# Kernel tuning notes

Measured on AMD Instinct MI355X. Metric: run time of the kernel, lower is better.

Reference implementation:

```python
import jax, jax.numpy as jnp
import numpy as np

N_NODES = 10000
N_EDGES = 160000
D = 128        # embedding_dim = in/out channels
E_DIM = 32     # edge feature dim
HEADS = 3
N_ETYPES = 64
ROUNDS = 2     # num_message_rounds
NEG_SLOPE = 0.2


def _lookup_maxnorm(table, idx):
    # torch Embedding(max_norm=1): rows with L2 norm > 1 are renormalized to norm 1
    v = table[idx]
    n = jnp.linalg.norm(v, axis=-1, keepdims=True)
    return v / jnp.maximum(n, 1.0)


def _edge_gat(x, src, dst, edge_attr, weight, att, euw, bias):
    # x: [N, D]; src/dst: [E] (self loops included); edge_attr: [E, E_DIM]
    N = x.shape[0]
    H = HEADS
    C = weight.shape[1] // H
    xh = (x @ weight).reshape(N, H, C)                 # [N, H, C]
    x_j = xh[src]                                      # gather source nodes  [E, H, C]
    x_i = xh[dst]                                      # gather target nodes  [E, H, C]
    ea = jnp.broadcast_to(edge_attr[:, None, :], (src.shape[0], H, edge_attr.shape[-1]))
    xj_cat = jnp.concatenate([x_j, ea], axis=-1)       # [E, H, C+E_DIM]
    # attention logits: (cat(x_i, x_j, e) * att).sum(-1)
    alpha = jnp.sum(jnp.concatenate([x_i, xj_cat], axis=-1) * att, axis=-1)  # [E, H]
    alpha = jax.nn.leaky_relu(alpha, NEG_SLOPE)
    # scatter-softmax over incoming edges of each dst node (stable)
    m = jax.ops.segment_max(alpha, dst, num_segments=N)        # [N, H]
    a = jnp.exp(alpha - m[dst])
    denom = jax.ops.segment_sum(a, dst, num_segments=N)        # [N, H]
    a = a / denom[dst]
    # weighted scatter-add aggregate
    aggr = jax.ops.segment_sum(xj_cat * a[..., None], dst, num_segments=N)  # [N, H, C+E_DIM]
    return aggr.mean(axis=1) @ euw + bias                       # [N, C]


def setup_inputs() -> dict:
    key = jax.random.key(0)
    ks = jax.random.split(key, 13)
    x_idx = jnp.arange(N_NODES, dtype=jnp.int32)
    src = jax.random.randint(ks[0], (N_EDGES,), 0, N_NODES, dtype=jnp.int32)
    off = jax.random.randint(ks[1], (N_EDGES,), 1, N_NODES, dtype=jnp.int32)
    dst = (src + off) % N_NODES    # guaranteed self-loop-free
    edge_index = jnp.stack([src, dst])
    edge_attr_idx = jax.random.randint(ks[2], (N_EDGES,), 0, N_ETYPES, dtype=jnp.int32)
    def g(k, shape):
        return jax.random.normal(k, shape, jnp.float32) * np.float32(np.sqrt(2.0 / sum(shape)))
    node_emb = g(ks[3], (N_NODES, D))
    edge_emb = g(ks[4], (N_ETYPES, E_DIM))
    w1 = g(ks[5], (D, HEADS * D))
    att1 = g(ks[6], (1, HEADS, 2 * D + E_DIM))
    euw1 = g(ks[7], (D + E_DIM, D))
    b1 = jnp.zeros((D,), jnp.float32)
    w2 = g(ks[8], (D, HEADS * D))
    att2 = g(ks[9], (1, HEADS, 2 * D + E_DIM))
    euw2 = g(ks[10], (D + E_DIM, D))
    b2 = jnp.zeros((D,), jnp.float32)
    return dict(x_idx=x_idx, edge_index=edge_index, edge_attr_idx=edge_attr_idx,
                node_emb=node_emb, edge_emb=edge_emb,
                w1=w1, att1=att1, euw1=euw1, b1=b1,
                w2=w2, att2=att2, euw2=euw2, b2=b2)


def reference(x_idx, edge_index, edge_attr_idx, node_emb, edge_emb,
              w1, att1, euw1, b1, w2, att2, euw2, b2):
    N = node_emb.shape[0]
    src0, dst0 = edge_index[0], edge_index[1]
    loop = jnp.arange(N, dtype=src0.dtype)
    src = jnp.concatenate([src0, loop])
    dst = jnp.concatenate([dst0, loop])
    x = _lookup_maxnorm(node_emb, x_idx)               # [N, D]
    ea = edge_emb[edge_attr_idx]                       # [E0, E_DIM]
    ea_full = jnp.concatenate([ea, jnp.zeros((N, ea.shape[-1]), ea.dtype)], axis=0)
    for _ in range(ROUNDS):
        # eval mode: dropout is identity
        x = jax.nn.elu(_edge_gat(x, src, dst, ea_full, w1, att1, euw1, b1))
        x = _edge_gat(x, src, dst, ea_full, w2, att2, euw2, b2)
    return x
```

## Files before the change

kernel.cpp:

```cpp
#include <hip/hip_runtime.h>
#include <hip/hip_bf16.h>

typedef __hip_bfloat16 bf16;
typedef __attribute__((ext_vector_type(8))) short short8;
typedef __attribute__((ext_vector_type(4))) float f32x4;

__device__ __forceinline__ float b2f(bf16 v) { return __bfloat162float(v); }
__device__ __forceinline__ float2 i2f2(int w) {
  float lo = __uint_as_float(((unsigned)w) << 16);
  float hi = __uint_as_float(((unsigned)w) & 0xFFFF0000u);
  return make_float2(lo, hi);
}
__device__ __forceinline__ unsigned f2bfb(float f) {
  unsigned u = __float_as_uint(f);
  unsigned r = 0x7FFFu + ((u >> 16) & 1u);
  return (u + r) >> 16;
}
__device__ __forceinline__ unsigned pk2(float a, float b) {
  return f2bfb(a) | (f2bfb(b) << 16);
}
__device__ __forceinline__ float ldv(const void* p, int i, int f) {
  return f ? ((const float*)p)[i] : b2f(((const bf16*)p)[i]);
}

__global__ __launch_bounds__(512) void detect_set_kernel(
    const unsigned short* __restrict__ probe, int nhalves, int* __restrict__ flag,
    const void* __restrict__ eeraw, const void* __restrict__ att1raw,
    const void* __restrict__ att2raw, float* __restrict__ s_et) {
  __shared__ int cnt;
  __shared__ int fl;
  if (threadIdx.x == 0) cnt = 0;
  __syncthreads();
  int local = 0;
  for (int i = threadIdx.x; i < nhalves; i += 512) {
    int e = (probe[i] >> 7) & 0xFF;
    if (e >= 160) local++;
  }
  if (local) atomicAdd(&cnt, local);
  __syncthreads();
  if (threadIdx.x == 0) { fl = (cnt > 16) ? 1 : 0; *flag = fl; }
  __syncthreads();
  int f = fl;
  int id = threadIdx.x;
  if (id < 2 * 65 * 3) {
    int l = id / (65 * 3);
    int r = id % (65 * 3);
    int t = r / 3, h = r % 3;
    const void* att = l ? att2raw : att1raw;
    float s = 0.0f;
    if (t < 64) {
      for (int d = 0; d < 32; ++d)
        s += ldv(eeraw, t * 32 + d, f) * ldv(att, h * 288 + 256 + d, f);
    }
    s_et[id] = s;
  }
}

__global__ __launch_bounds__(256) void wconv_kernel(
    const void* __restrict__ ee, const void* __restrict__ w1,
    const void* __restrict__ a1, const void* __restrict__ eu1,
    const void* __restrict__ b1, const void* __restrict__ w2,
    const void* __restrict__ a2, const void* __restrict__ eu2,
    const void* __restrict__ b2, const int* __restrict__ flag,
    float* __restrict__ eef, float* __restrict__ att1f, float* __restrict__ att2f,
    float* __restrict__ b1f, float* __restrict__ b2f,
    bf16* __restrict__ WT1, bf16* __restrict__ WT2,
    bf16* __restrict__ euT1, bf16* __restrict__ euT2,
    int* __restrict__ counts, int N) {
  int i = blockIdx.x * 256 + threadIdx.x;
  int f = *flag;
  if (i < 2048) {
    eef[i] = ldv(ee, i, f);
  } else if (i < 2912) {
    att1f[i - 2048] = ldv(a1, i - 2048, f);
  } else if (i < 3776) {
    att2f[i - 2912] = ldv(a2, i - 2912, f);
  } else if (i < 3904) {
    b1f[i - 3776] = ldv(b1, i - 3776, f);
  } else if (i < 4032) {
    b2f[i - 3904] = ldv(b2, i - 3904, f);
  } else if (i < 53184) {
    int j = i - 4032; int c = j >> 7, k = j & 127;
    WT1[j] = __float2bfloat16(ldv(w1, k * 384 + c, f));
  } else if (i < 102336) {
    int j = i - 53184; int c = j >> 7, k = j & 127;
    WT2[j] = __float2bfloat16(ldv(w2, k * 384 + c, f));
  } else if (i < 122816) {
    int j = i - 102336; int c = j / 160, k = j % 160;
    euT1[j] = __float2bfloat16(ldv(eu1, k * 128 + c, f));
  } else if (i < 143296) {
    int j = i - 122816; int c = j / 160, k = j % 160;
    euT2[j] = __float2bfloat16(ldv(eu2, k * 128 + c, f));
  } else if (i < 143296 + N) {
    counts[i - 143296] = 0;
  }
}

__global__ __launch_bounds__(256) void prep_kernel(
    const int* __restrict__ x_idx, const void* __restrict__ node_emb,
    const int* __restrict__ flag, bf16* __restrict__ xb,
    int* __restrict__ counts, const int* __restrict__ dst, int E0, int N) {
  int wid = threadIdx.x >> 6, lane = threadIdx.x & 63;
  int n = blockIdx.x * 4 + wid;
  if (n < N) {
    int idx = x_idx[n];
    if ((unsigned)idx >= (unsigned)N) idx = 0;
    float v0, v1;
    if (*flag) {
      const float* er = (const float*)node_emb + (size_t)idx * 128;
      v0 = er[lane]; v1 = er[lane + 64];
    } else {
      const bf16* er = (const bf16*)node_emb + (size_t)idx * 128;
      v0 = b2f(er[lane]); v1 = b2f(er[lane + 64]);
    }
    float ss = v0 * v0 + v1 * v1;
#pragma unroll
    for (int d = 32; d > 0; d >>= 1) ss += __shfl_xor(ss, d);
    float norm = sqrtf(ss);
    float scale = norm > 1.0f ? 1.0f / norm : 1.0f;
    xb[(size_t)n * 128 + lane] = __float2bfloat16(v0 * scale);
    xb[(size_t)n * 128 + 64 + lane] = __float2bfloat16(v1 * scale);
  }
  int gid = blockIdx.x * 256 + threadIdx.x;
  int stride = gridDim.x * 256;
  for (int i = gid; i < E0; i += stride) {
    int d = dst[i];
    if ((unsigned)d >= (unsigned)N) d = 0;
    atomicAdd(&counts[d], 1);
  }
}

__global__ __launch_bounds__(64) void scan_kernel(
    int* __restrict__ counts, int* __restrict__ row_ptr, int N) {
  int lane = threadIdx.x;
  int chunk = (N + 63) / 64;
  int lo = lane * chunk;
  int hi = lo + chunk; if (hi > N) hi = N; if (lo > N) lo = N;
  int s = 0;
  for (int i = lo; i < hi; ++i) s += counts[i] + 1;
  int incl = s;
#pragma unroll
  for (int d = 1; d < 64; d <<= 1) {
    int t = __shfl_up(incl, d);
    if (lane >= d) incl += t;
  }
  int run = incl - s;
  for (int i = lo; i < hi; ++i) {
    int c = counts[i] + 1;
    row_ptr[i] = run;
    counts[i] = run;
    run += c;
  }
  if (lane == 63) row_ptr[N] = run;
}

__global__ __launch_bounds__(256) void scatter_kernel(
    const int* __restrict__ src, const int* __restrict__ dst,
    const int* __restrict__ et, int* __restrict__ cursor,
    int* __restrict__ packed, int E0, int N) {
  int E = E0 + N;
  int i = blockIdx.x * blockDim.x + threadIdx.x;
  if (i < E0) {
    int d = dst[i];
    if ((unsigned)d >= (unsigned)N) d = 0;
    int p = atomicAdd(&cursor[d], 1);
    if ((unsigned)p >= (unsigned)E) p = 0;
    int t = et[i] & 63;
    packed[p] = (src[i] & 0xFFFF) | (t << 16);
  } else if (i < E) {
    int n = i - E0;
    int p = atomicAdd(&cursor[n], 1);
    if ((unsigned)p >= (unsigned)E) p = 0;
    packed[p] = (n & 0xFFFF) | (64 << 16);
  }
}

__global__ __launch_bounds__(256) void gemm_xh_mfma(
    const bf16* __restrict__ x, const bf16* __restrict__ WT,
    bf16* __restrict__ xh, int N) {
  int wave = threadIdx.x >> 6, lane = threadIdx.x & 63;
  int row_base = blockIdx.x * 16;
  int col_base = blockIdx.y * 64 + wave * 16;
  int quad = lane >> 4, r16 = lane & 15;
  int row = row_base + r16; if (row >= N) row = N - 1;
  int col = col_base + r16;
  f32x4 acc = {0.f, 0.f, 0.f, 0.f};
  const short8* ap = (const short8*)(x + (size_t)row * 128 + quad * 8);
  const short8* bp = (const short8*)(WT + (size_t)col * 128 + quad * 8);
#pragma unroll
  for (int kk = 0; kk < 4; ++kk) {
    short8 a = ap[kk * 4];
    short8 b = bp[kk * 4];
    acc = __builtin_amdgcn_mfma_f32_16x16x32_bf16(a, b, acc, 0, 0, 0);
  }
  int h = col >> 7, fi = col & 127, pair = fi >> 1, sub = fi & 1;
  size_t base = (size_t)pair * 6 + h * 2 + sub;
#pragma unroll
  for (int r = 0; r < 4; ++r) {
    int node = row_base + quad * 4 + r;
    if (node < N) xh[(size_t)node * 384 + base] = __float2bfloat16(acc[r]);
  }
}

__global__ __launch_bounds__(256) void s_kernel(
    const int* __restrict__ xh_i, const float2* __restrict__ attf2,
    float* __restrict__ s_i, float* __restrict__ s_j, int N) {
  int wid = threadIdx.x >> 6, lane = threadIdx.x & 63;
  int n = blockIdx.x * 4 + wid;
  if (n >= N) return;
  const int* p = xh_i + (size_t)n * 192 + lane * 3;
  int w0 = p[0], w1 = p[1], w2 = p[2];
  float2 v[3] = {i2f2(w0), i2f2(w1), i2f2(w2)};
#pragma unroll
  for (int h = 0; h < 3; ++h) {
    float2 ai = attf2[h * 144 + lane];
    float2 aj = attf2[h * 144 + 64 + lane];
    float pi = v[h].x * ai.x + v[h].y * ai.y;
    float pj = v[h].x * aj.x + v[h].y * aj.y;
#pragma unroll
    for (int d = 32; d > 0; d >>= 1) {
      pi += __shfl_xor(pi, d);
      pj += __shfl_xor(pj, d);
    }
    if (lane == 0) {
      s_i[n * 3 + h] = pi;
      s_j[n * 3 + h] = pj;
    }
  }
}

__global__ __launch_bounds__(256) void edge_aggr_kernel(
    const int* __restrict__ xh_i, const float* __restrict__ s_i,
    const float* __restrict__ s_j, const float* __restrict__ s_et,
    const float2* __restrict__ eef2, const int* __restrict__ row_ptr,
    const int* __restrict__ packed, unsigned* __restrict__ aggr_u,
    int N, int E) {
  int wid = threadIdx.x >> 6, lane = threadIdx.x & 63;
  int n = blockIdx.x * 4 + wid;
  if (n >= N) return;
  int start = row_ptr[n], end = row_ptr[n + 1];
  if (start < 0) start = 0;
  if (start > E) start = E;
  if (end < start) end = start;
  if (end > E) end = E;
  int deg = end - start;
  float si0 = s_i[n * 3 + 0], si1 = s_i[n * 3 + 1], si2 = s_i[n * 3 + 2];

  float p0r[2], p1r[2], p2r[2];
  int pkr[2];
  float dp0 = 0.0f, dp1 = 0.0f, dp2 = 0.0f;
#pragma unroll
  for (int it = 0; it < 2; ++it) {
    p0r[it] = p1r[it] = p2r[it] = 0.0f; pkr[it] = 0;
    int slot = it * 64 + lane;
    if (slot < deg) {
      int p = packed[start + slot];
      int s = p & 0xFFFF; if (s >= N) s = N - 1;
      int t = (p >> 16) & 127; if (t > 64) t = 64;
      float a0 = si0 + s_j[s * 3 + 0] + s_et[t * 3 + 0];
      float a1 = si1 + s_j[s * 3 + 1] + s_et[t * 3 + 1];
      float a2 = si2 + s_j[s * 3 + 2] + s_et[t * 3 + 2];
      a0 = a0 > 0.0f ? a0 : 0.2f * a0;
      a1 = a1 > 0.0f ? a1 : 0.2f * a1;
      a2 = a2 > 0.0f ? a2 : 0.2f * a2;
      a0 = fminf(fmaxf(a0, -60.0f), 60.0f);
      a1 = fminf(fmaxf(a1, -60.0f), 60.0f);
      a2 = fminf(fmaxf(a2, -60.0f), 60.0f);
      float p0 = __expf(a0), p1 = __expf(a1), p2 = __expf(a2);
      dp0 += p0; dp1 += p1; dp2 += p2;
      p0r[it] = p0; p1r[it] = p1; p2r[it] = p2;
      pkr[it] = s | (t << 16);
    }
  }
#pragma unroll
  for (int d = 32; d > 0; d >>= 1) {
    dp0 += __shfl_xor(dp0, d);
    dp1 += __shfl_xor(dp1, d);
    dp2 += __shfl_xor(dp2, d);
  }
  float d0 = dp0, d1 = dp1, d2 = dp2;

  float2 ax0 = make_float2(0.f, 0.f), ax1 = ax0, ax2 = ax0;
  float2 ae0 = ax0, ae1 = ax0, ae2 = ax0;
  int mm = deg < 128 ? deg : 128;

  auto agg_range = [&](int pk_s, float q0_s, float q1_s, float q2_s, int cnt) {
    int j = 0;
    for (; j + 2 <= cnt; j += 2) {
      int pkA = __shfl(pk_s, j), pkB = __shfl(pk_s, j + 1);
      float qA0 = __shfl(q0_s, j), qB0 = __shfl(q0_s, j + 1);
      float qA1 = __shfl(q1_s, j), qB1 = __shfl(q1_s, j + 1);
      float qA2 = __shfl(q2_s, j), qB2 = __shfl(q2_s, j + 1);
      int sA = pkA & 0xFFFF, tA = pkA >> 16;
      int sB = pkB & 0xFFFF, tB = pkB >> 16;
      const int* xpA = xh_i + (size_t)sA * 192 + lane * 3;
      const int* xpB = xh_i + (size_t)sB * 192 + lane * 3;
      int wA0 = xpA[0], wA1 = xpA[1], wA2 = xpA[2];
      int wB0 = xpB[0], wB1 = xpB[1], wB2 = xpB[2];
      float2 vA0 = i2f2(wA0), vA1 = i2f2(wA1), vA2 = i2f2(wA2);
      float2 vB0 = i2f2(wB0), vB1 = i2f2(wB1), vB2 = i2f2(wB2);
      ax0.x = fmaf(qA0, vA0.x, ax0.x); ax0.y = fmaf(qA0, vA0.y, ax0.y);
      ax1.x = fmaf(qA1, vA1.x, ax1.x); ax1.y = fmaf(qA1, vA1.y, ax1.y);
      ax2.x = fmaf(qA2, vA2.x, ax2.x); ax2.y = fmaf(qA2, vA2.y, ax2.y);
      ax0.x = fmaf(qB0, vB0.x, ax0.x); ax0.y = fmaf(qB0, vB0.y, ax0.y);
      ax1.x = fmaf(qB1, vB1.x, ax1.x); ax1.y = fmaf(qB1, vB1.y, ax1.y);
      ax2.x = fmaf(qB2, vB2.x, ax2.x); ax2.y = fmaf(qB2, vB2.y, ax2.y);
      if (lane < 16) {
        if (tA != 64) {
          float2 ev = eef2[tA * 16 + lane];
          ae0.x = fmaf(qA0, ev.x, ae0.x); ae0.y = fmaf(qA0, ev.y, ae0.y);
          ae1.x = fmaf(qA1, ev.x, ae1.x); ae1.y = fmaf(qA1, ev.y, ae1.y);
          ae2.x = fmaf(qA2, ev.x, ae2.x); ae2.y = fmaf(qA2, ev.y, ae2.y);
        }
        if (tB != 64) {
          float2 ev = eef2[tB * 16 + lane];
          ae0.x = fmaf(qB0, ev.x, ae0.x); ae0.y = fmaf(qB0, ev.y, ae0.y);
          ae1.x = fmaf(qB1, ev.x, ae1.x); ae1.y = fmaf(qB1, ev.y, ae1.y);
          ae2.x = fmaf(qB2, ev.x, ae2.x); ae2.y = fmaf(qB2, ev.y, ae2.y);
        }
      }
    }
    if (j < cnt) {
      int pkA = __shfl(pk_s, j);
      float qA0 = __shfl(q0_s, j), qA1 = __shfl(q1_s, j), qA2 = __shfl(q2_s, j);
      int sA = pkA & 0xFFFF, tA = pkA >> 16;
      const int* xpA = xh_i + (size_t)sA * 192 + lane * 3;
      int wA0 = xpA[0], wA1 = xpA[1], wA2 = xpA[2];
      float2 vA0 = i2f2(wA0), vA1 = i2f2(wA1), vA2 = i2f2(wA2);
      ax0.x = fmaf(qA0, vA0.x, ax0.x); ax0.y = fmaf(qA0, vA0.y, ax0.y);
      ax1.x = fmaf(qA1, vA1.x, ax1.x); ax1.y = fmaf(qA1, vA1.y, ax1.y);
      ax2.x = fmaf(qA2, vA2.x, ax2.x); ax2.y = fmaf(qA2, vA2.y, ax2.y);
      if (lane < 16 && tA != 64) {
        float2 ev = eef2[tA * 16 + lane];
        ae0.x = fmaf(qA0, ev.x, ae0.x); ae0.y = fmaf(qA0, ev.y, ae0.y);
        ae1.x = fmaf(qA1, ev.x, ae1.x); ae1.y = fmaf(qA1, ev.y, ae1.y);
        ae2.x = fmaf(qA2, ev.x, ae2.x); ae2.y = fmaf(qA2, ev.y, ae2.y);
      }
    }
  };
  agg_range(pkr[0], p0r[0], p1r[0], p2r[0], mm < 64 ? mm : 64);
  if (mm > 64) agg_range(pkr[1], p0r[1], p1r[1], p2r[1], mm - 64);

  for (int e = start + 128; e < end; ++e) {
    int p = packed[e];
    int s = p & 0xFFFF; if (s >= N) s = N - 1;
    int t = (p >> 16) & 127; if (t > 64) t = 64;
    float a0 = si0 + s_j[s * 3 + 0] + s_et[t * 3 + 0];
    float a1 = si1 + s_j[s * 3 + 1] + s_et[t * 3 + 1];
    float a2 = si2 + s_j[s * 3 + 2] + s_et[t * 3 + 2];
    a0 = a0 > 0.0f ? a0 : 0.2f * a0;
    a1 = a1 > 0.0f ? a1 : 0.2f * a1;
    a2 = a2 > 0.0f ? a2 : 0.2f * a2;
    a0 = fminf(fmaxf(a0, -60.0f), 60.0f);
    a1 = fminf(fmaxf(a1, -60.0f), 60.0f);
    a2 = fminf(fmaxf(a2, -60.0f), 60.0f);
    float p0 = __expf(a0), p1 = __expf(a1), p2 = __expf(a2);
    d0 += p0; d1 += p1; d2 += p2;
    const int* xp = xh_i + (size_t)s * 192 + lane * 3;
    float2 v0 = i2f2(xp[0]), v1 = i2f2(xp[1]), v2 = i2f2(xp[2]);
    ax0.x = fmaf(p0, v0.x, ax0.x); ax0.y = fmaf(p0, v0.y, ax0.y);
    ax1.x = fmaf(p1, v1.x, ax1.x); ax1.y = fmaf(p1, v1.y, ax1.y);
    ax2.x = fmaf(p2, v2.x, ax2.x); ax2.y = fmaf(p2, v2.y, ax2.y);
    if (t != 64 && lane < 16) {
      float2 ev = eef2[t * 16 + lane];
      ae0.x = fmaf(p0, ev.x, ae0.x); ae0.y = fmaf(p0, ev.y, ae0.y);
      ae1.x = fmaf(p1, ev.x, ae1.x); ae1.y = fmaf(p1, ev.y, ae1.y);
      ae2.x = fmaf(p2, ev.x, ae2.x); ae2.y = fmaf(p2, ev.y, ae2.y);
    }
  }

  const float third = 1.0f / 3.0f;
  float i0 = third / fmaxf(d0, 1e-30f);
  float i1 = third / fmaxf(d1, 1e-30f);
  float i2 = third / fmaxf(d2, 1e-30f);
  aggr_u[(size_t)n * 80 + lane] =
      pk2(ax0.x * i0 + ax1.x * i1 + ax2.x * i2,
          ax0.y * i0 + ax1.y * i1 + ax2.y * i2);
  if (lane < 16)
    aggr_u[(size_t)n * 80 + 64 + lane] =
        pk2(ae0.x * i0 + ae1.x * i1 + ae2.x * i2,
            ae0.y * i0 + ae1.y * i1 + ae2.y * i2);
}

__global__ __launch_bounds__(256) void gemm_out_mfma(
    const bf16* __restrict__ aggr, const bf16* __restrict__ euwT,
    const float* __restrict__ biasf, bf16* __restrict__ xb,
    void* __restrict__ dout, const int* __restrict__ flag,
    int N, int do_elu, int do_final) {
  int wave = threadIdx.x >> 6, lane = threadIdx.x & 63;
  int row_base = blockIdx.x * 16;
  int col_base = blockIdx.y * 64 + wave * 16;
  int quad = lane >> 4, r16 = lane & 15;
  int row = row_base + r16; if (row >= N) row = N - 1;
  int col = col_base + r16;
  f32x4 acc = {0.f, 0.f, 0.f, 0.f};
  const short8* ap = (const short8*)(aggr + (size_t)row * 160 + quad * 8);
  const short8* bp = (const short8*)(euwT + (size_t)col * 160 + quad * 8);
#pragma unroll
  for (int kk = 0; kk < 5; ++kk) {
    short8 a = ap[kk * 4];
    short8 b = bp[kk * 4];
    acc = __builtin_amdgcn_mfma_f32_16x16x32_bf16(a, b, acc, 0, 0, 0);
  }
  float bv = biasf[col];
  int f = *flag;
#pragma unroll
  for (int r = 0; r < 4; ++r) {
    int node = row_base + quad * 4 + r;
    if (node < N) {
      float v = acc[r] + bv;
      if (do_elu) v = v > 0.0f ? v : expm1f(v);
      if (do_final) {
        if (f) ((float*)dout)[(size_t)node * 128 + col] = v;
        else   ((bf16*)dout)[(size_t)node * 128 + col] = __float2bfloat16(v);
      } else {
        xb[(size_t)node * 128 + col] = __float2bfloat16(v);
      }
    }
  }
}

extern "C" void kernel_launch(void* const* d_in, const int* in_sizes, int n_in,
                              void* d_out, int out_size, void* d_ws, size_t ws_size,
                              hipStream_t stream) {
  const int* x_idx = (const int*)d_in[0];
  const int* edge_index = (const int*)d_in[1];
  const int* edge_attr_idx = (const int*)d_in[2];

  int N = in_sizes[0];
  int E0 = in_sizes[1] / 2;
  int E = E0 + N;
  const int* src = edge_index;
  const int* dst = edge_index + E0;

  size_t off = 0;
  char* base = (char*)d_ws;
  auto carve = [&](size_t bytes) -> void* {
    void* p = base + off;
    off += (bytes + 255) & ~(size_t)255;
    return p;
  };
  int* flag     = (int*)carve(256);
  int* counts   = (int*)carve((size_t)N * 4);
  int* row_ptr  = (int*)carve((size_t)(N + 1) * 4);
  int* packed   = (int*)carve((size_t)E * 4);
  float* s_i    = (float*)carve((size_t)N * 3 * 4);
  float* s_j    = (float*)carve((size_t)N * 3 * 4);
  float* s_et   = (float*)carve(2 * 65 * 3 * 4);
  float* eef    = (float*)carve(2048 * 4);
  float* att1f  = (float*)carve(864 * 4);
  float* att2f  = (float*)carve(864 * 4);
  float* b1f    = (float*)carve(128 * 4);
  float* b2f_   = (float*)carve(128 * 4);
  bf16* WT1     = (bf16*)carve(49152 * 2);
  bf16* WT2     = (bf16*)carve(49152 * 2);
  bf16* euT1    = (bf16*)carve(20480 * 2);
  bf16* euT2    = (bf16*)carve(20480 * 2);
  bf16* xh      = (bf16*)carve((size_t)N * 384 * 2 + 64);
  bf16* aggr    = (bf16*)carve((size_t)N * 160 * 2);
  bf16* xb      = (bf16*)d_out;
  (void)n_in; (void)out_size; (void)ws_size;

  detect_set_kernel<<<1, 512, 0, stream>>>(
      (const unsigned short*)d_in[5], 2048, flag, d_in[4], d_in[6], d_in[10], s_et);
  wconv_kernel<<<(143296 + N + 255) / 256, 256, 0, stream>>>(
      d_in[4], d_in[5], d_in[6], d_in[7], d_in[8], d_in[9], d_in[10], d_in[11],
      d_in[12], flag, eef, att1f, att2f, b1f, b2f_, WT1, WT2, euT1, euT2,
      counts, N);
  int nb4 = (N + 3) / 4;
  prep_kernel<<<nb4, 256, 0, stream>>>(x_idx, d_in[3], flag, xb, counts, dst,
                                       E0, N);
  scan_kernel<<<1, 64, 0, stream>>>(counts, row_ptr, N);
  scatter_kernel<<<(E + 255) / 256, 256, 0, stream>>>(src, dst, edge_attr_idx,
                                                      counts, packed, E0, N);

  const bf16* WTs[2] = {WT1, WT2};
  const float* atts[2] = {att1f, att2f};
  const bf16* euTs[2] = {euT1, euT2};
  const float* bs[2] = {b1f, b2f_};

  int nrb = (N + 15) / 16;
  for (int round = 0; round < 2; ++round) {
    for (int l = 0; l < 2; ++l) {
      int do_elu = (l == 0) ? 1 : 0;
      int do_final = (round == 1 && l == 1) ? 1 : 0;
      gemm_xh_mfma<<<dim3(nrb, 6), 256, 0, stream>>>(xb, WTs[l], xh, N);
      s_kernel<<<nb4, 256, 0, stream>>>((const int*)xh, (const float2*)atts[l],
                                        s_i, s_j, N);
      edge_aggr_kernel<<<nb4, 256, 0, stream>>>(
          (const int*)xh, s_i, s_j, s_et + l * 195, (const float2*)eef,
          row_ptr, packed, (unsigned*)aggr, N, E);
      gemm_out_mfma<<<dim3(nrb, 2), 256, 0, stream>>>(
          aggr, euTs[l], bs[l], xb, d_out, flag, N, do_elu, do_final);
    }
  }
}
```

Measured before the change: 382.0 us.

## Fuse attention score computation into xh GEMM and widen scan to 1024 threads

Merges the per-node attention dot products (s_i, s_j) into the xh projection GEMM epilogue, computing partial sums from MFMA accumulators and reducing via shuffles and LDS. This removes a separate kernel launch and a re-read of xh per layer. It also parallelizes the single-block prefix scan from 64 to 1024 threads with a two-level wave scan. The GEMM now uses one 384-thread block per 16 rows, which gives fewer blocks and lower parallelism, and it computes the scores from fp32 accumulators rather than the rounded bf16 values.

```diff
diff --git a/kernel.cpp b/kernel.cpp
--- a/kernel.cpp
+++ b/kernel.cpp
@@ -130,28 +130,40 @@
   }
 }
 
-__global__ __launch_bounds__(64) void scan_kernel(
+__global__ __launch_bounds__(1024) void scan_kernel(
     int* __restrict__ counts, int* __restrict__ row_ptr, int N) {
-  int lane = threadIdx.x;
-  int chunk = (N + 63) / 64;
-  int lo = lane * chunk;
-  int hi = lo + chunk; if (hi > N) hi = N; if (lo > N) lo = N;
+  __shared__ int wsum[16];
+  int t = threadIdx.x;
+  int chunk = (N + 1023) >> 10;
+  int lo = t * chunk;
+  int hi = lo + chunk;
+  if (lo > N) lo = N;
+  if (hi > N) hi = N;
   int s = 0;
   for (int i = lo; i < hi; ++i) s += counts[i] + 1;
+  int lane = t & 63, wv = t >> 6;
   int incl = s;
 #pragma unroll
   for (int d = 1; d < 64; d <<= 1) {
-    int t = __shfl_up(incl, d);
-    if (lane >= d) incl += t;
-  }
-  int run = incl - s;
+    int u = __shfl_up(incl, d);
+    if (lane >= d) incl += u;
+  }
+  if (lane == 63) wsum[wv] = incl;
+  __syncthreads();
+  if (t == 0) {
+    int run = 0;
+#pragma unroll
+    for (int w = 0; w < 16; ++w) { int c = wsum[w]; wsum[w] = run; run += c; }
+  }
+  __syncthreads();
+  int run = incl - s + wsum[wv];
   for (int i = lo; i < hi; ++i) {
     int c = counts[i] + 1;
     row_ptr[i] = run;
     counts[i] = run;
     run += c;
   }
-  if (lane == 63) row_ptr[N] = run;
+  if (t == 1023) row_ptr[N] = run;
 }
 
 __global__ __launch_bounds__(256) void scatter_kernel(
@@ -175,57 +187,72 @@
   }
 }
 
-__global__ __launch_bounds__(256) void gemm_xh_mfma(
+__global__ __launch_bounds__(384) void gemm_xh_s_mfma(
     const bf16* __restrict__ x, const bf16* __restrict__ WT,
-    bf16* __restrict__ xh, int N) {
+    const float* __restrict__ attf, bf16* __restrict__ xh,
+    float* __restrict__ s_i, float* __restrict__ s_j, int N) {
+  __shared__ float lds_i[6][16];
+  __shared__ float lds_j[6][16];
   int wave = threadIdx.x >> 6, lane = threadIdx.x & 63;
   int row_base = blockIdx.x * 16;
-  int col_base = blockIdx.y * 64 + wave * 16;
   int quad = lane >> 4, r16 = lane & 15;
   int row = row_base + r16; if (row >= N) row = N - 1;
-  int col = col_base + r16;
-  f32x4 acc = {0.f, 0.f, 0.f, 0.f};
   const short8* ap = (const short8*)(x + (size_t)row * 128 + quad * 8);
-  const short8* bp = (const short8*)(WT + (size_t)col * 128 + quad * 8);
-#pragma unroll
-  for (int kk = 0; kk < 4; ++kk) {
-    short8 a = ap[kk * 4];
-    short8 b = bp[kk * 4];
-    acc = __builtin_amdgcn_mfma_f32_16x16x32_bf16(a, b, acc, 0, 0, 0);
-  }
-  int h = col >> 7, fi = col & 127, pair = fi >> 1, sub = fi & 1;
-  size_t base = (size_t)pair * 6 + h * 2 + sub;
-#pragma unroll
-  for (int r = 0; r < 4; ++r) {
-    int node = row_base + quad * 4 + r;
-    if (node < N) xh[(size_t)node * 384 + base] = __float2bfloat16(acc[r]);
-  }
-}
-
-__global__ __launch_bounds__(256) void s_kernel(
-    const int* __restrict__ xh_i, const float2* __restrict__ attf2,
-    float* __restrict__ s_i, float* __restrict__ s_j, int N) {
-  int wid = threadIdx.x >> 6, lane = threadIdx.x & 63;
-  int n = blockIdx.x * 4 + wid;
-  if (n >= N) return;
-  const int* p = xh_i + (size_t)n * 192 + lane * 3;
-  int w0 = p[0], w1 = p[1], w2 = p[2];
-  float2 v[3] = {i2f2(w0), i2f2(w1), i2f2(w2)};
-#pragma unroll
-  for (int h = 0; h < 3; ++h) {
-    float2 ai = attf2[h * 144 + lane];
-    float2 aj = attf2[h * 144 + 64 + lane];
-    float pi = v[h].x * ai.x + v[h].y * ai.y;
-    float pj = v[h].x * aj.x + v[h].y * aj.y;
-#pragma unroll
-    for (int d = 32; d > 0; d >>= 1) {
-      pi += __shfl_xor(pi, d);
-      pj += __shfl_xor(pj, d);
-    }
-    if (lane == 0) {
-      s_i[n * 3 + h] = pi;
-      s_j[n * 3 + h] = pj;
-    }
+  short8 a[4];
+#pragma unroll
+  for (int kk = 0; kk < 4; ++kk) a[kk] = ap[kk * 4];
+
+  float pi_r[4] = {0.f, 0.f, 0.f, 0.f};
+  float pj_r[4] = {0.f, 0.f, 0.f, 0.f};
+#pragma unroll
+  for (int j = 0; j < 4; ++j) {
+    int col = wave * 64 + j * 16 + r16;
+    const short8* bp = (const short8*)(WT + (size_t)col * 128 + quad * 8);
+    f32x4 acc = {0.f, 0.f, 0.f, 0.f};
+#pragma unroll
+    for (int kk = 0; kk < 4; ++kk)
+      acc = __builtin_amdgcn_mfma_f32_16x16x32_bf16(a[kk], bp[kk * 4], acc, 0, 0, 0);
+    int h = col >> 7, fi = col & 127, pair = fi >> 1, sub = fi & 1;
+    size_t base = (size_t)pair * 6 + h * 2 + sub;
+#pragma unroll
+    for (int r = 0; r < 4; ++r) {
+      int node = row_base + quad * 4 + r;
+      if (node < N) xh[(size_t)node * 384 + base] = __float2bfloat16(acc[r]);
+    }
+    float ai = attf[h * 288 + fi];
+    float aj = attf[h * 288 + 128 + fi];
+#pragma unroll
+    for (int r = 0; r < 4; ++r) {
+      pi_r[r] = fmaf(acc[r], ai, pi_r[r]);
+      pj_r[r] = fmaf(acc[r], aj, pj_r[r]);
+    }
+  }
+#pragma unroll
+  for (int d = 1; d < 16; d <<= 1) {
+#pragma unroll
+    for (int r = 0; r < 4; ++r) {
+      pi_r[r] += __shfl_xor(pi_r[r], d);
+      pj_r[r] += __shfl_xor(pj_r[r], d);
+    }
+  }
+  if (r16 == 0) {
+#pragma unroll
+    for (int r = 0; r < 4; ++r) {
+      lds_i[wave][quad * 4 + r] = pi_r[r];
+      lds_j[wave][quad * 4 + r] = pj_r[r];
+    }
+  }
+  __syncthreads();
+  int m = threadIdx.x;
+  if (m < 48) {
+    int h = m / 16, r = m % 16;
+    int node = row_base + r;
+    if (node < N) s_i[node * 3 + h] = lds_i[2 * h][r] + lds_i[2 * h + 1][r];
+  } else if (m < 96) {
+    int tt = m - 48;
+    int h = tt / 16, r = tt % 16;
+    int node = row_base + r;
+    if (node < N) s_j[node * 3 + h] = lds_j[2 * h][r] + lds_j[2 * h + 1][r];
   }
 }
 
@@ -470,7 +497,7 @@
   int nb4 = (N + 3) / 4;
   prep_kernel<<<nb4, 256, 0, stream>>>(x_idx, d_in[3], flag, xb, counts, dst,
                                        E0, N);
-  scan_kernel<<<1, 64, 0, stream>>>(counts, row_ptr, N);
+  scan_kernel<<<1, 1024, 0, stream>>>(counts, row_ptr, N);
   scatter_kernel<<<(E + 255) / 256, 256, 0, stream>>>(src, dst, edge_attr_idx,
                                                       counts, packed, E0, N);
 
@@ -484,9 +511,8 @@
     for (int l = 0; l < 2; ++l) {
       int do_elu = (l == 0) ? 1 : 0;
       int do_final = (round == 1 && l == 1) ? 1 : 0;
-      gemm_xh_mfma<<<dim3(nrb, 6), 256, 0, stream>>>(xb, WTs[l], xh, N);
-      s_kernel<<<nb4, 256, 0, stream>>>((const int*)xh, (const float2*)atts[l],
-                                        s_i, s_j, N);
+      gemm_xh_s_mfma<<<nrb, 384, 0, stream>>>(xb, WTs[l], atts[l], xh,
+                                              s_i, s_j, N);
       edge_aggr_kernel<<<nb4, 256, 0, stream>>>(
           (const int*)xh, s_i, s_j, s_et + l * 195, (const float2*)eef,
           row_ptr, packed, (unsigned*)aggr, N, E);
```

After: 328.6 us. -14.0%, faster.
